# Performance work log

Hardware: AMD Instinct MI355X
Metric: run time of the kernel (lower is better)

## Reference

```python
import math
import jax, jax.numpy as jnp
import numpy as np
from jax.scipy.special import erf

BATCH, SEQ, DIM = 2, 4096, 128
EMA_HEADS, DQK, DV = 16, 64, 256
NUM_BUCKETS, MAX_DIST = 32, 128


def _next_fast_len(n):
    # smallest 5-smooth integer >= n (matches scipy.fftpack.next_fast_len)
    while True:
        m = n
        for p in (2, 3, 5):
            while m % p == 0:
                m //= p
        if m == 1:
            return n
        n += 1


def _laplacian_attn(x):
    mu = math.sqrt(0.5)
    std = math.sqrt(0.25 * math.pi)
    return 0.5 * (1.0 + erf((x - mu) / (std * math.sqrt(2.0))))


def _rel_pos_bias(table, n, scale):
    # causal T5 relative position bias, bucket(q_pos - k_pos)
    pos = jnp.arange(n)
    rel = jnp.maximum(pos[:, None] - pos[None, :], 0)  # [n, n], >= 0
    max_exact = NUM_BUCKETS // 2
    is_small = rel < max_exact
    val_large = max_exact + (
        jnp.log(jnp.maximum(rel, 1).astype(jnp.float32) / max_exact)
        / math.log(MAX_DIST / max_exact) * (NUM_BUCKETS - max_exact)
    ).astype(jnp.int32)
    val_large = jnp.minimum(val_large, NUM_BUCKETS - 1)
    bucket = jnp.where(is_small, rel, val_large)
    return table[bucket, 0] * scale  # [n, n]


def _conv1d_fft(x, K, n):
    # x: [b, n, h, d] (fft over axis 1), K: [n, h] (fft over axis 0)
    fast_len = _next_fast_len(2 * n - 1)
    f_x = jnp.fft.rfft(x, n=fast_len, axis=1)
    f_K = jnp.fft.rfft(K, n=fast_len, axis=0)
    out = jnp.fft.irfft(f_x * jnp.conj(f_K)[None, :, :, None], fast_len, axis=1)
    out = jnp.roll(out, -1, axis=1)
    return out[:, fast_len - n:]  # [b, n, h, d]


def _forward(x, expansion, reduction, alphas, dampen, Wqk, bqk, gamma, beta,
             Wv, bv, rel_table, Wr, br, Wu, bu, Wh, Uh, bh):
    b, n, d = x.shape
    # ---- multi-headed EMA (causal -> unidirectional) via FFT conv ----
    xe = jnp.einsum('bnd,hd->bnhd', x, expansion)
    a = jax.nn.sigmoid(alphas)            # [h]
    dm = jax.nn.sigmoid(dampen)           # [h]
    powers = jnp.arange(n - 1, -1, -1, dtype=x.dtype)  # reversed powers
    K = a * ((1.0 - a) * dm) ** powers[:, None]        # [n, h]
    conv = _conv1d_fft(xe, K, n)
    ema = jnp.einsum('bnhd,hd->bnd', conv, reduction)  # [b, n, d]
    # ---- single-headed attention (chunk_size=-1 -> one chunk), v from x ----
    qk = jax.nn.silu(ema @ Wqk + bqk)     # [b, n, dqk]
    q = qk * gamma[0] + beta[0]
    k = qk * gamma[1] + beta[1]
    v = jax.nn.silu(x @ Wv + bv)          # [b, n, dv]
    scale = 1.0 / n                       # laplacian_attn_fn scaling
    sim = jnp.einsum('bid,bjd->bij', q, k) * scale
    sim = sim + _rel_pos_bias(rel_table, n, DQK ** 0.5)
    attn = _laplacian_attn(sim)
    causal_mask = jnp.triu(jnp.ones((n, n), dtype=bool), 1)
    attn = jnp.where(causal_mask, 0.0, attn)  # laplacian: zero after activation
    attn_out = jnp.einsum('bij,bjd->bid', attn, v)  # [b, n, dv]
    # ---- gating + output ----
    reset_gate = jax.nn.silu(ema @ Wr + br)         # [b, n, dv]
    update_gate = jax.nn.sigmoid(ema @ Wu + bu)     # [b, n, d]
    gated = attn_out * reset_gate
    H = jax.nn.silu(ema @ Wh + gated @ Uh + bh)     # [b, n, d]
    return update_gate * H + (1.0 - update_gate) * x


def setup_inputs() -> dict:
    key = jax.random.key(0)
    ks = jax.random.split(key, 18)
    def rn(i, shape, s=1.0):
        return jax.random.normal(ks[i], shape, dtype=jnp.float32) * s
    return dict(
        x=rn(0, (BATCH, SEQ, DIM)),
        expansion=rn(1, (EMA_HEADS, DIM), 0.2),
        reduction=rn(2, (EMA_HEADS, DIM), 0.2),
        alphas=rn(3, (EMA_HEADS,)),
        dampen=rn(4, (EMA_HEADS,)),
        Wqk=rn(5, (DIM, DQK), 0.05), bqk=rn(6, (DQK,), 0.02),
        gamma=rn(7, (2, DQK), 0.02), beta=jnp.zeros((2, DQK), jnp.float32),
        Wv=rn(8, (DIM, DV), 0.05), bv=rn(9, (DV,), 0.02),
        rel_table=rn(10, (NUM_BUCKETS, 1), 0.02),
        Wr=rn(11, (DIM, DV), 0.05), br=rn(12, (DV,), 0.02),
        Wu=rn(13, (DIM, DIM), 0.05), bu=rn(14, (DIM,), 0.02),
        Wh=rn(15, (DIM, DIM), 0.05), Uh=rn(16, (DV, DIM), 0.05),
        bh=rn(17, (DIM,), 0.02),
    )


def reference(x, expansion, reduction, alphas, dampen, Wqk, bqk, gamma, beta,
              Wv, bv, rel_table, Wr, br, Wu, bu, Wh, Uh, bh):
    return _forward(x, expansion, reduction, alphas, dampen, Wqk, bqk, gamma,
                    beta, Wv, bv, rel_table, Wr, br, Wu, bu, Wh, Uh, bh)
```

## Files before the change

### kernel.cpp

```cpp
#include <hip/hip_runtime.h>
#include <cstdint>
#include <cmath>

#define B_ 2
#define N_ 4096
#define D_ 128
#define H_ 16
#define DQK_ 64
#define DV_ 256

typedef float    f4_t  __attribute__((ext_vector_type(4)));
typedef float    f16f  __attribute__((ext_vector_type(16)));
typedef _Float16 h4_t  __attribute__((ext_vector_type(4)));
typedef _Float16 h8_t  __attribute__((ext_vector_type(8)));

__device__ __forceinline__ float sigmoidf_(float z) { return 1.f/(1.f + expf(-z)); }
__device__ __forceinline__ float siluf_(float z)    { return z/(1.f + expf(-z)); }
__device__ __forceinline__ f16f zero16() {
  f16f z;
#pragma unroll
  for (int i = 0; i < 16; ++i) z[i] = 0.f;
  return z;
}

__global__ void ema_phase1(const float* __restrict__ x, const float* __restrict__ expansion,
                           const float* __restrict__ alphas, const float* __restrict__ dampen,
                           float* __restrict__ F, _Float16* __restrict__ xh) {
  int bid = blockIdx.x;
  int dg = bid & 7, c = (bid >> 3) & 63, b = bid >> 9;
  int h = threadIdx.x & 15, dl = threadIdx.x >> 4;
  int d = dg*16 + dl;
  float a  = sigmoidf_(alphas[h]);
  float dm = sigmoidf_(dampen[h]);
  float q  = (1.f - a)*dm;
  float coef = a * expansion[h*D_ + d];
  __shared__ float xs[64][16];
  {
    int e = threadIdx.x;
    int t = e >> 2, seg = e & 3;
    const float* xp = x + ((size_t)b*N_ + c*64 + t)*D_ + dg*16 + seg*4;
    f4_t v = *(const f4_t*)xp;
    *(f4_t*)&xs[t][seg*4] = v;
    h4_t hv;
#pragma unroll
    for (int j = 0; j < 4; ++j) hv[j] = (_Float16)v[j];
    *(h4_t*)(xh + ((size_t)b*N_ + c*64 + t)*D_ + dg*16 + seg*4) = hv;
  }
  __syncthreads();
  float s = 0.f;
#pragma unroll
  for (int t = 0; t < 64; ++t) s = fmaf(q, s, coef*xs[t][dl]);
  F[(((size_t)b*H_ + h)*D_ + d)*64 + c] = s;
}

__global__ void ema_carry(const float* __restrict__ F, const float* __restrict__ alphas,
                          const float* __restrict__ dampen, float* __restrict__ carry) {
  int idx = blockIdx.x*256 + threadIdx.x;
  int h = (idx >> 7) & 15;
  float a  = sigmoidf_(alphas[h]);
  float dm = sigmoidf_(dampen[h]);
  float q  = (1.f - a)*dm;
  float qL = q;
#pragma unroll
  for (int i = 0; i < 6; ++i) qL *= qL;
  const float* Fp = F + (size_t)idx*64;
  float* cp = carry + (size_t)idx*64;
  float s = 0.f;
  for (int cc = 0; cc < 64; ++cc) { cp[cc] = s; s = fmaf(qL, s, Fp[cc]); }
}

__global__ void ema_phase2(const float* __restrict__ x, const float* __restrict__ expansion,
                           const float* __restrict__ reduction,
                           const float* __restrict__ alphas, const float* __restrict__ dampen,
                           const float* __restrict__ carry, _Float16* __restrict__ emah) {
  int bid = blockIdx.x;
  int dg = bid & 7, c = (bid >> 3) & 63, b = bid >> 9;
  int h = threadIdx.x & 15, dl = threadIdx.x >> 4;
  int d = dg*16 + dl;
  float a  = sigmoidf_(alphas[h]);
  float dm = sigmoidf_(dampen[h]);
  float q  = (1.f - a)*dm;
  float coef = a * expansion[h*D_ + d];
  float red  = reduction[h*D_ + d];
  __shared__ float xs[64][16];
  {
    int e = threadIdx.x;
    int t = e >> 2, seg = e & 3;
    const float* xp = x + ((size_t)b*N_ + c*64 + t)*D_ + dg*16 + seg*4;
    *(f4_t*)&xs[t][seg*4] = *(const f4_t*)xp;
  }
  __syncthreads();
  float s = carry[(((size_t)b*H_ + h)*D_ + d)*64 + c];
  for (int t = 0; t < 64; ++t) {
    s = fmaf(q, s, coef*xs[t][dl]);
    float v = red * s;
    v += __shfl_xor(v, 1); v += __shfl_xor(v, 2);
    v += __shfl_xor(v, 4); v += __shfl_xor(v, 8);
    if (h == 0) emah[((size_t)b*N_ + c*64 + t)*D_ + d] = (_Float16)v;
  }
}

__global__ void prep_all(const float* __restrict__ Wqk, const float* __restrict__ Wv,
                         const float* __restrict__ Wr, const float* __restrict__ Wu,
                         const float* __restrict__ Wh,
                         const float* __restrict__ bqk, const float* __restrict__ bv,
                         const float* __restrict__ br, const float* __restrict__ bu,
                         const float* __restrict__ bh,
                         const float* __restrict__ Uh, const float* __restrict__ rel_table,
                         _Float16* __restrict__ Wt, float* __restrict__ bcat,
                         _Float16* __restrict__ Uht, float* __restrict__ bias2T) {
  int idx = blockIdx.x*256 + threadIdx.x;
  if (idx < 832*128) {
    int c = idx >> 7, d = idx & 127;
    const float* W; const float* bias; int ncol, cl;
    if (c < 64)       { W=Wqk; bias=bqk; ncol=64;  cl=c; }
    else if (c < 320) { W=Wv;  bias=bv;  ncol=256; cl=c-64; }
    else if (c < 576) { W=Wr;  bias=br;  ncol=256; cl=c-320; }
    else if (c < 704) { W=Wu;  bias=bu;  ncol=128; cl=c-576; }
    else              { W=Wh;  bias=bh;  ncol=128; cl=c-704; }
    Wt[idx] = (_Float16)W[d*ncol + cl];
    if (d == 0) bcat[c] = bias[cl];
  } else if (idx < 832*128 + 32768) {
    int i2 = idx - 832*128;
    int k = i2 >> 7, c = i2 & 127;
    Uht[(size_t)c*256 + k] = (_Float16)Uh[i2];
  } else if (idx < 832*128 + 32768 + 4096) {
    int r = idx - (832*128 + 32768);
    int bucket;
    if (r < 16) bucket = r;
    else {
      double v = log((double)r / 16.0) / log(8.0) * 16.0;
      bucket = 16 + (int)v;
      if (bucket > 31) bucket = 31;
    }
    bias2T[r] = (rel_table[bucket]*8.0f - 0.70710678f) * 1.1283792f;
  }
}

__global__ __launch_bounds__(256) void linear_mfma(
    const _Float16* __restrict__ emah, const _Float16* __restrict__ xh,
    const _Float16* __restrict__ Wt, const float* __restrict__ bcat,
    const float* __restrict__ gamma, const float* __restrict__ beta,
    _Float16* __restrict__ qh, _Float16* __restrict__ kh, _Float16* __restrict__ vTt,
    float* __restrict__ resetb, float* __restrict__ updateb, float* __restrict__ hemab) {
  int slab = blockIdx.x % 13, rt = blockIdx.x / 13;
  int tid = threadIdx.x;
  int lane = tid & 63, w = tid >> 6;
  int lr = lane & 15, lg = lane >> 4;
  int mode = (slab==0)?0:(slab<5)?1:(slab<9)?2:(slab<11)?3:4;
  const _Float16* src = (mode==1) ? xh : emah;
  __shared__ _Float16 As[64][136];
  __shared__ _Float16 Ws[64][136];
  {
    const h8_t* s8 = (const h8_t*)(src + (size_t)rt*64*D_);
#pragma unroll
    for (int i = 0; i < 4; ++i) {
      int idx = tid + i*256;
      int row = idx >> 4, seg = idx & 15;
      *(h8_t*)&As[row][seg*8] = s8[idx];
    }
    const h8_t* w8 = (const h8_t*)(Wt + (size_t)slab*64*D_);
#pragma unroll
    for (int i = 0; i < 4; ++i) {
      int idx = tid + i*256;
      int row = idx >> 4, seg = idx & 15;
      *(h8_t*)&Ws[row][seg*8] = w8[idx];
    }
  }
  __syncthreads();
  h4_t af[8];
#pragma unroll
  for (int ks = 0; ks < 8; ++ks) af[ks] = *(const h4_t*)&As[w*16 + lr][ks*16 + lg*4];
  int row0 = rt*64 + w*16 + lg*4;
#pragma unroll
  for (int ns = 0; ns < 4; ++ns) {
    f4_t acc = (f4_t){0.f,0.f,0.f,0.f};
#pragma unroll
    for (int ks = 0; ks < 8; ++ks) {
      h4_t bf = *(const h4_t*)&Ws[ns*16 + lr][ks*16 + lg*4];
      acc = __builtin_amdgcn_mfma_f32_16x16x16f16(af[ks], bf, acc, 0, 0, 0);
    }
    int c = slab*64 + ns*16 + lr;
    float bias = bcat[c];
    if (mode == 0) {
      float g0 = gamma[c], g1 = gamma[64+c], be0 = beta[c], be1 = beta[64+c];
#pragma unroll
      for (int r = 0; r < 4; ++r) {
        float qk = siluf_(acc[r] + bias);
        size_t row = row0 + r;
        qh[row*DQK_ + c] = (_Float16)(qk*g0 + be0);
        kh[row*DQK_ + c] = (_Float16)(qk*g1 + be1);
      }
    } else if (mode == 1) {
      int cl = c - 64;
      int bb = row0 >> 12, rl = row0 & 4095;
      h4_t vv;
#pragma unroll
      for (int r = 0; r < 4; ++r) vv[r] = (_Float16)siluf_(acc[r] + bias);
      *(h4_t*)&vTt[(((size_t)bb*128 + (rl>>5))*256 + cl)*32 + (rl&31)] = vv;
    } else if (mode == 2) {
      int cl = c - 320;
#pragma unroll
      for (int r = 0; r < 4; ++r) resetb[(size_t)(row0 + r)*DV_ + cl] = siluf_(acc[r] + bias);
    } else if (mode == 3) {
      int cl = c - 576;
#pragma unroll
      for (int r = 0; r < 4; ++r) updateb[(size_t)(row0 + r)*D_ + cl] = sigmoidf_(acc[r] + bias);
    } else {
      int cl = c - 704;
#pragma unroll
      for (int r = 0; r < 4; ++r) hemab[(size_t)(row0 + r)*D_ + cl] = acc[r] + bias;
    }
  }
}

__global__ __launch_bounds__(256, 3) void attn_kernel(
    const _Float16* __restrict__ qh, const _Float16* __restrict__ kh,
    const _Float16* __restrict__ vTt, const float* __restrict__ bias2T,
    _Float16* __restrict__ attnp) {
  int bid = blockIdx.x;
  int it = 63 - (bid >> 5);
  int rem = bid & 31;
  int s = rem >> 1, b = rem & 1;
  int a = it >> 2, r = it & 3;
  int nblk = a + 1;
  if (s >= nblk) return;
  int T = 2*it + 2;
  int tlo = (s*T)/nblk, thi = ((s+1)*T)/nblk;
  int nt = thi - tlo;
  int base = it + 2*a*(a-1) + r*a;
  int slot = base + s;
  int i0 = it * 64;
  int tid = threadIdx.x;
  int lane = tid & 63, w = tid >> 6;
  int ih = w & 1;
  int dvh = w >> 1;
  bool prod = (dvh == 0);
  int lm = lane & 31, lg = lane >> 5;

  __shared__ __align__(16) char Vb[2][18432];
  __shared__ __align__(16) char Kb[2][4352];
  __shared__ __align__(16) char Pb[2][2560];
  __shared__ float biasW[320];

  int jmaxv = thi*32 - 1;
  int dlo = i0 - jmaxv;
  int cnt = 64 + jmaxv - tlo*32;
  for (int k = tid; k < cnt; k += 256) {
    int d = dlo + k;
    biasW[k] = d < 0 ? -1e38f : bias2T[d];
  }

  h4_t qf[8];
  if (prod) {
    const _Float16* qp = qh + ((size_t)b*N_ + i0 + ih*32 + lm)*DQK_ + 4*lg;
#pragma unroll
    for (int ksq = 0; ksq < 8; ++ksq) qf[ksq] = *(const h4_t*)(qp + 8*ksq);
  }

  f16f accO[4];
#pragma unroll
  for (int i = 0; i < 4; ++i) accO[i] = zero16();

  const _Float16* kbase = kh + (size_t)b*N_*DQK_;
  const _Float16* vbase = vTt + (size_t)b*128*8192;
  int st = tid & 127;
  int kr = st >> 2, ks16 = st & 3;

  h8_t k8a, k8b, vr[8];
#define ISSUE_(JT) { \
  const _Float16* kp_ = kbase + (size_t)((JT)*32 + kr)*DQK_ + ks16*16; \
  k8a = *(const h8_t*)kp_; k8b = *(const h8_t*)(kp_ + 8); \
  const _Float16* vp_ = vbase + (size_t)(JT)*8192 + st*32; \
  _Pragma("unroll") for (int i = 0; i < 4; ++i) vr[i] = *(const h8_t*)(vp_ + i*8); \
  _Pragma("unroll") for (int i = 0; i < 4; ++i) vr[4+i] = *(const h8_t*)(vp_ + 4096 + i*8); }

#define COMMIT_(BI) { \
  char* kb_ = Kb[BI] + kr*136 + ks16*32; \
  *(h4_t*)kb_        = __builtin_shufflevector(k8a, k8a, 0,1,2,3); \
  *(h4_t*)(kb_ + 8)  = __builtin_shufflevector(k8a, k8a, 4,5,6,7); \
  *(h4_t*)(kb_ + 16) = __builtin_shufflevector(k8b, k8b, 0,1,2,3); \
  *(h4_t*)(kb_ + 24) = __builtin_shufflevector(k8b, k8b, 4,5,6,7); \
  char* va_ = Vb[BI] + st*72; \
  _Pragma("unroll") for (int i = 0; i < 4; ++i) { \
    *(h4_t*)(va_ + i*16)     = __builtin_shufflevector(vr[i], vr[i], 0,1,2,3); \
    *(h4_t*)(va_ + i*16 + 8) = __builtin_shufflevector(vr[i], vr[i], 4,5,6,7); } \
  char* vb2_ = Vb[BI] + (st + 128)*72; \
  _Pragma("unroll") for (int i = 0; i < 4; ++i) { \
    *(h4_t*)(vb2_ + i*16)     = __builtin_shufflevector(vr[4+i], vr[4+i], 0,1,2,3); \
    *(h4_t*)(vb2_ + i*16 + 8) = __builtin_shufflevector(vr[4+i], vr[4+i], 4,5,6,7); } }

  if (!prod) {
    ISSUE_(tlo);
    COMMIT_(0);
    if (nt > 1) ISSUE_(tlo + 1);
  }
  __syncthreads();

  const float C1 = 1.1283792f / 4096.f;
  int ibase = i0 + ih*32 + lm;
#pragma unroll 1
  for (int t = 0; t < nt; ++t) {
    h4_t pa[4];
    if (prod) {
      const char* kb = Kb[t & 1];
      __builtin_amdgcn_s_setprio(1);
      f16f accS = zero16();
#pragma unroll
      for (int ksq = 0; ksq < 8; ++ksq) {
        h4_t kf = *(const h4_t*)(kb + lm*136 + 16*ksq + 8*lg);
        accS = __builtin_amdgcn_mfma_f32_32x32x8f16(kf, qf[ksq], accS, 0, 0, 0);
      }
      __builtin_amdgcn_s_setprio(0);
      int idx0 = ibase - dlo - (tlo + t)*32 - 4*lg;
#pragma unroll
      for (int rr = 0; rr < 16; ++rr) {
        float tt = fmaf(accS[rr], C1, biasW[idx0 - 8*(rr>>2) - (rr&3)]);
        float e = tt*fmaf(tt*tt, -0.101797f, -2.304877f);
        float u = exp2f(e);
        float pv = __builtin_amdgcn_rcpf(1.f + u);
        pa[rr>>2][rr&3] = (_Float16)pv;
      }
      char* pp = Pb[ih] + lane*40;
#pragma unroll
      for (int k2 = 0; k2 < 4; ++k2) *(h4_t*)(pp + k2*8) = pa[k2];
    } else {
      if (t+1 < nt) COMMIT_((t+1) & 1);
      if (t+2 < nt) ISSUE_(tlo + t + 2);
    }
    __syncthreads();
    if (!prod) {
      const char* pp = Pb[ih] + lane*40;
#pragma unroll
      for (int k2 = 0; k2 < 4; ++k2) pa[k2] = *(const h4_t*)(pp + k2*8);
    }
    const char* vb = Vb[t & 1];
    __builtin_amdgcn_s_setprio(1);
#pragma unroll
    for (int ks = 0; ks < 4; ++ks) {
#pragma unroll
      for (int dvb = 0; dvb < 4; ++dvb) {
        h4_t vf = *(const h4_t*)(vb + (dvh*128 + dvb*32 + lm)*72 + 16*ks + 8*lg);
        accO[dvb] = __builtin_amdgcn_mfma_f32_32x32x8f16(pa[ks], vf, accO[dvb], 0, 0, 0);
      }
    }
    __builtin_amdgcn_s_setprio(0);
    __syncthreads();
  }
#undef ISSUE_
#undef COMMIT_

  _Float16* op = attnp + ((size_t)b*544 + slot)*(64*256);
#pragma unroll
  for (int dvb = 0; dvb < 4; ++dvb) {
    int col = dvh*128 + dvb*32 + lm;
#pragma unroll
    for (int rr = 0; rr < 16; ++rr) {
      int row = ih*32 + 8*(rr>>2) + 4*lg + (rr&3);
      op[(size_t)row*256 + col] = (_Float16)accO[dvb][rr];
    }
  }
}

__global__ void combine_gated(const _Float16* __restrict__ attnp, const float* __restrict__ resetb,
                              _Float16* __restrict__ gatedh) {
  size_t fi = (size_t)blockIdx.x*256 + threadIdx.x;
  int c4 = (int)(fi & 63);
  int rr = (int)(fi >> 6);
  int b = rr >> 12, n = rr & 4095;
  int it = n >> 6, rowLocal = n & 63;
  int a = it >> 2, r = it & 3;
  int nblk = a + 1;
  int base = it + 2*a*(a-1) + r*a;
  const _Float16* ap = attnp + ((size_t)b*544 + base)*16384 + rowLocal*256 + c4*4;
  f4_t acc = (f4_t){0.f,0.f,0.f,0.f};
  for (int s2 = 0; s2 < nblk; ++s2) {
    h4_t pv = *(const h4_t*)(ap + (size_t)s2*16384);
#pragma unroll
    for (int j = 0; j < 4; ++j) acc[j] += (float)pv[j];
  }
  f4_t rg = ((const f4_t*)resetb)[fi];
  f4_t g = acc * rg;
  h4_t hg;
#pragma unroll
  for (int j = 0; j < 4; ++j) hg[j] = (_Float16)g[j];
  *(h4_t*)(gatedh + fi*4) = hg;
}

__global__ __launch_bounds__(256) void final_mfma(
    const _Float16* __restrict__ gatedh, const _Float16* __restrict__ Uht,
    const float* __restrict__ hemab, const float* __restrict__ updateb,
    const float* __restrict__ x, float* __restrict__ out) {
  int rt = blockIdx.x >> 1, cs = blockIdx.x & 1;
  int tid = threadIdx.x;
  int lane = tid & 63, w = tid >> 6;
  int lr = lane & 15, lg = lane >> 4;
  int row0 = rt*64, c0 = cs*64;
  __shared__ _Float16 As[64][136];
  __shared__ _Float16 Ws[64][136];
  f4_t acc[4];
#pragma unroll
  for (int ns = 0; ns < 4; ++ns) acc[ns] = (f4_t){0.f,0.f,0.f,0.f};
#pragma unroll
  for (int kc = 0; kc < 2; ++kc) {
    __syncthreads();
#pragma unroll
    for (int i = 0; i < 4; ++i) {
      int idx = tid + i*256;
      int row = idx >> 4, seg = idx & 15;
      *(h8_t*)&As[row][seg*8] =
          *(const h8_t*)(gatedh + (size_t)(row0 + row)*DV_ + kc*128 + seg*8);
      *(h8_t*)&Ws[row][seg*8] =
          *(const h8_t*)(Uht + (size_t)(c0 + row)*DV_ + kc*128 + seg*8);
    }
    __syncthreads();
    h4_t af[8];
#pragma unroll
    for (int ks = 0; ks < 8; ++ks) af[ks] = *(const h4_t*)&As[w*16 + lr][ks*16 + lg*4];
#pragma unroll
    for (int ns = 0; ns < 4; ++ns) {
#pragma unroll
      for (int ks = 0; ks < 8; ++ks) {
        h4_t bf = *(const h4_t*)&Ws[ns*16 + lr][ks*16 + lg*4];
        acc[ns] = __builtin_amdgcn_mfma_f32_16x16x16f16(af[ks], bf, acc[ns], 0, 0, 0);
      }
    }
  }
  int orow = row0 + w*16 + lg*4;
#pragma unroll
  for (int ns = 0; ns < 4; ++ns) {
    int col = c0 + ns*16 + lr;
#pragma unroll
    for (int r = 0; r < 4; ++r) {
      size_t o = (size_t)(orow + r)*D_ + col;
      float z = acc[ns][r] + hemab[o];
      float Hv = siluf_(z);
      float u  = updateb[o];
      out[o] = u*Hv + (1.f - u)*x[o];
    }
  }
}

extern "C" void kernel_launch(void* const* d_in, const int* in_sizes, int n_in,
                              void* d_out, int out_size, void* d_ws, size_t ws_size,
                              hipStream_t stream) {
  (void)in_sizes; (void)n_in; (void)out_size; (void)ws_size;
  const float* x         = (const float*)d_in[0];
  const float* expansion = (const float*)d_in[1];
  const float* reduction = (const float*)d_in[2];
  const float* alphas    = (const float*)d_in[3];
  const float* dampen    = (const float*)d_in[4];
  const float* Wqk       = (const float*)d_in[5];
  const float* bqk       = (const float*)d_in[6];
  const float* gamma     = (const float*)d_in[7];
  const float* beta      = (const float*)d_in[8];
  const float* Wv        = (const float*)d_in[9];
  const float* bv        = (const float*)d_in[10];
  const float* rel_table = (const float*)d_in[11];
  const float* Wr        = (const float*)d_in[12];
  const float* br        = (const float*)d_in[13];
  const float* Wu        = (const float*)d_in[14];
  const float* bu        = (const float*)d_in[15];
  const float* Wh        = (const float*)d_in[16];
  const float* Uh        = (const float*)d_in[17];
  const float* bh        = (const float*)d_in[18];
  float* out = (float*)d_out;

  char* p = (char*)d_ws;
  size_t off = 0;
  auto alloc = [&](size_t bytes) -> char* {
    char* r = p + off;
    off += (bytes + 255) & ~(size_t)255;
    return r;
  };
  float*    F      = (float*)alloc((size_t)B_*H_*D_*64*4);
  float*    carry  = (float*)alloc((size_t)B_*H_*D_*64*4);
  _Float16* emah   = (_Float16*)alloc((size_t)B_*N_*D_*2);
  _Float16* xh     = (_Float16*)alloc((size_t)B_*N_*D_*2);
  float*    bias2T = (float*)alloc((size_t)N_*4);
  _Float16* Wt     = (_Float16*)alloc((size_t)832*128*2);
  float*    bcat   = (float*)alloc((size_t)832*4);
  _Float16* Uht    = (_Float16*)alloc((size_t)D_*DV_*2);
  _Float16* qh     = (_Float16*)alloc((size_t)B_*N_*DQK_*2);
  _Float16* kh     = (_Float16*)alloc((size_t)B_*N_*DQK_*2);
  _Float16* vTt    = (_Float16*)alloc((size_t)B_*DV_*N_*2);
  float*    resetb = (float*)alloc((size_t)B_*N_*DV_*4);
  float*    updateb= (float*)alloc((size_t)B_*N_*D_*4);
  float*    hemab  = (float*)alloc((size_t)B_*N_*D_*4);
  _Float16* gatedh = (_Float16*)alloc((size_t)B_*N_*DV_*2);
  _Float16* attnp  = (_Float16*)alloc((size_t)B_*544*64*256*2);

  prep_all<<<560, 256, 0, stream>>>(Wqk, Wv, Wr, Wu, Wh, bqk, bv, br, bu, bh,
                                    Uh, rel_table, Wt, bcat, Uht, bias2T);
  ema_phase1<<<1024, 256, 0, stream>>>(x, expansion, alphas, dampen, F, xh);
  ema_carry<<<16, 256, 0, stream>>>(F, alphas, dampen, carry);
  ema_phase2<<<1024, 256, 0, stream>>>(x, expansion, reduction, alphas, dampen, carry, emah);
  linear_mfma<<<128*13, 256, 0, stream>>>(emah, xh, Wt, bcat, gamma, beta,
                                          qh, kh, vTt, resetb, updateb, hemab);
  attn_kernel<<<2048, 256, 0, stream>>>(qh, kh, vTt, bias2T, attnp);
  combine_gated<<<2048, 256, 0, stream>>>(attnp, resetb, gatedh);
  final_mfma<<<256, 256, 0, stream>>>(gatedh, Uht, hemab, updateb, x, out);
}
```

Measured before the change: 113.8 us.

## Parallelize EMA carry with warp scan; store reset/update gates as fp16

The sequential per-thread carry recurrence over 64 chunks, run on only 16 blocks, is replaced by a wave-level Hillis-Steele scan over the affine recurrence, launched on 1024 blocks with one wave per (b,h,d) row. This removes a long serial dependency chain with low occupancy. Separately, the reset and update gate buffers are stored in fp16 instead of fp32, halving their write and read traffic in linear_mfma, combine_gated and final_mfma. The cost is some precision loss in the gate values and a different summation order in the carry.

```diff
diff --git a/kernel.cpp b/kernel.cpp
--- a/kernel.cpp
+++ b/kernel.cpp
@@ -55,18 +55,25 @@
 
 __global__ void ema_carry(const float* __restrict__ F, const float* __restrict__ alphas,
                           const float* __restrict__ dampen, float* __restrict__ carry) {
-  int idx = blockIdx.x*256 + threadIdx.x;
-  int h = (idx >> 7) & 15;
+  int wid = blockIdx.x*4 + (threadIdx.x >> 6);
+  int lane = threadIdx.x & 63;
+  int h = (wid >> 7) & 15;
   float a  = sigmoidf_(alphas[h]);
   float dm = sigmoidf_(dampen[h]);
   float q  = (1.f - a)*dm;
   float qL = q;
 #pragma unroll
   for (int i = 0; i < 6; ++i) qL *= qL;
-  const float* Fp = F + (size_t)idx*64;
-  float* cp = carry + (size_t)idx*64;
-  float s = 0.f;
-  for (int cc = 0; cc < 64; ++cc) { cp[cc] = s; s = fmaf(qL, s, Fp[cc]); }
+  float A = qL;
+  float Bv = F[(size_t)wid*64 + lane];
+#pragma unroll
+  for (int len = 1; len < 64; len <<= 1) {
+    float Ap = __shfl_up(A, len);
+    float Bp = __shfl_up(Bv, len);
+    if (lane >= len) { Bv = fmaf(A, Bp, Bv); A = A*Ap; }
+  }
+  float Bprev = __shfl_up(Bv, 1);
+  carry[(size_t)wid*64 + lane] = (lane == 0) ? 0.f : Bprev;
 }
 
 __global__ void ema_phase2(const float* __restrict__ x, const float* __restrict__ expansion,
@@ -142,7 +149,8 @@
     const _Float16* __restrict__ Wt, const float* __restrict__ bcat,
     const float* __restrict__ gamma, const float* __restrict__ beta,
     _Float16* __restrict__ qh, _Float16* __restrict__ kh, _Float16* __restrict__ vTt,
-    float* __restrict__ resetb, float* __restrict__ updateb, float* __restrict__ hemab) {
+    _Float16* __restrict__ resetbh, _Float16* __restrict__ updatebh,
+    float* __restrict__ hemab) {
   int slab = blockIdx.x % 13, rt = blockIdx.x / 13;
   int tid = threadIdx.x;
   int lane = tid & 63, w = tid >> 6;
@@ -201,11 +209,13 @@
     } else if (mode == 2) {
       int cl = c - 320;
 #pragma unroll
-      for (int r = 0; r < 4; ++r) resetb[(size_t)(row0 + r)*DV_ + cl] = siluf_(acc[r] + bias);
+      for (int r = 0; r < 4; ++r)
+        resetbh[(size_t)(row0 + r)*DV_ + cl] = (_Float16)siluf_(acc[r] + bias);
     } else if (mode == 3) {
       int cl = c - 576;
 #pragma unroll
-      for (int r = 0; r < 4; ++r) updateb[(size_t)(row0 + r)*D_ + cl] = sigmoidf_(acc[r] + bias);
+      for (int r = 0; r < 4; ++r)
+        updatebh[(size_t)(row0 + r)*D_ + cl] = (_Float16)sigmoidf_(acc[r] + bias);
     } else {
       int cl = c - 704;
 #pragma unroll
@@ -362,7 +372,8 @@
   }
 }
 
-__global__ void combine_gated(const _Float16* __restrict__ attnp, const float* __restrict__ resetb,
+__global__ void combine_gated(const _Float16* __restrict__ attnp,
+                              const _Float16* __restrict__ resetbh,
                               _Float16* __restrict__ gatedh) {
   size_t fi = (size_t)blockIdx.x*256 + threadIdx.x;
   int c4 = (int)(fi & 63);
@@ -379,17 +390,16 @@
 #pragma unroll
     for (int j = 0; j < 4; ++j) acc[j] += (float)pv[j];
   }
-  f4_t rg = ((const f4_t*)resetb)[fi];
-  f4_t g = acc * rg;
+  h4_t rg = *(const h4_t*)(resetbh + fi*4);
   h4_t hg;
 #pragma unroll
-  for (int j = 0; j < 4; ++j) hg[j] = (_Float16)g[j];
+  for (int j = 0; j < 4; ++j) hg[j] = (_Float16)(acc[j] * (float)rg[j]);
   *(h4_t*)(gatedh + fi*4) = hg;
 }
 
 __global__ __launch_bounds__(256) void final_mfma(
     const _Float16* __restrict__ gatedh, const _Float16* __restrict__ Uht,
-    const float* __restrict__ hemab, const float* __restrict__ updateb,
+    const float* __restrict__ hemab, const _Float16* __restrict__ updatebh,
     const float* __restrict__ x, float* __restrict__ out) {
   int rt = blockIdx.x >> 1, cs = blockIdx.x & 1;
   int tid = threadIdx.x;
@@ -435,7 +445,7 @@
       size_t o = (size_t)(orow + r)*D_ + col;
       float z = acc[ns][r] + hemab[o];
       float Hv = siluf_(z);
-      float u  = updateb[o];
+      float u  = (float)updatebh[o];
       out[o] = u*Hv + (1.f - u)*x[o];
     }
   }
@@ -473,31 +483,31 @@
     off += (bytes + 255) & ~(size_t)255;
     return r;
   };
-  float*    F      = (float*)alloc((size_t)B_*H_*D_*64*4);
-  float*    carry  = (float*)alloc((size_t)B_*H_*D_*64*4);
-  _Float16* emah   = (_Float16*)alloc((size_t)B_*N_*D_*2);
-  _Float16* xh     = (_Float16*)alloc((size_t)B_*N_*D_*2);
-  float*    bias2T = (float*)alloc((size_t)N_*4);
-  _Float16* Wt     = (_Float16*)alloc((size_t)832*128*2);
-  float*    bcat   = (float*)alloc((size_t)832*4);
-  _Float16* Uht    = (_Float16*)alloc((size_t)D_*DV_*2);
-  _Float16* qh     = (_Float16*)alloc((size_t)B_*N_*DQK_*2);
-  _Float16* kh     = (_Float16*)alloc((size_t)B_*N_*DQK_*2);
-  _Float16* vTt    = (_Float16*)alloc((size_t)B_*DV_*N_*2);
-  float*    resetb = (float*)alloc((size_t)B_*N_*DV_*4);
-  float*    updateb= (float*)alloc((size_t)B_*N_*D_*4);
-  float*    hemab  = (float*)alloc((size_t)B_*N_*D_*4);
-  _Float16* gatedh = (_Float16*)alloc((size_t)B_*N_*DV_*2);
-  _Float16* attnp  = (_Float16*)alloc((size_t)B_*544*64*256*2);
+  float*    F       = (float*)alloc((size_t)B_*H_*D_*64*4);
+  float*    carry   = (float*)alloc((size_t)B_*H_*D_*64*4);
+  _Float16* emah    = (_Float16*)alloc((size_t)B_*N_*D_*2);
+  _Float16* xh      = (_Float16*)alloc((size_t)B_*N_*D_*2);
+  float*    bias2T  = (float*)alloc((size_t)N_*4);
+  _Float16* Wt      = (_Float16*)alloc((size_t)832*128*2);
+  float*    bcat    = (float*)alloc((size_t)832*4);
+  _Float16* Uht     = (_Float16*)alloc((size_t)D_*DV_*2);
+  _Float16* qh      = (_Float16*)alloc((size_t)B_*N_*DQK_*2);
+  _Float16* kh      = (_Float16*)alloc((size_t)B_*N_*DQK_*2);
+  _Float16* vTt     = (_Float16*)alloc((size_t)B_*DV_*N_*2);
+  _Float16* resetbh = (_Float16*)alloc((size_t)B_*N_*DV_*2);
+  _Float16* updatebh= (_Float16*)alloc((size_t)B_*N_*D_*2);
+  float*    hemab   = (float*)alloc((size_t)B_*N_*D_*4);
+  _Float16* gatedh  = (_Float16*)alloc((size_t)B_*N_*DV_*2);
+  _Float16* attnp   = (_Float16*)alloc((size_t)B_*544*64*256*2);
 
   prep_all<<<560, 256, 0, stream>>>(Wqk, Wv, Wr, Wu, Wh, bqk, bv, br, bu, bh,
                                     Uh, rel_table, Wt, bcat, Uht, bias2T);
   ema_phase1<<<1024, 256, 0, stream>>>(x, expansion, alphas, dampen, F, xh);
-  ema_carry<<<16, 256, 0, stream>>>(F, alphas, dampen, carry);
+  ema_carry<<<1024, 256, 0, stream>>>(F, alphas, dampen, carry);
   ema_phase2<<<1024, 256, 0, stream>>>(x, expansion, reduction, alphas, dampen, carry, emah);
   linear_mfma<<<128*13, 256, 0, stream>>>(emah, xh, Wt, bcat, gamma, beta,
-                                          qh, kh, vTt, resetb, updateb, hemab);
+                                          qh, kh, vTt, resetbh, updatebh, hemab);
   attn_kernel<<<2048, 256, 0, stream>>>(qh, kh, vTt, bias2T, attnp);
-  combine_gated<<<2048, 256, 0, stream>>>(attnp, resetb, gatedh);
-  final_mfma<<<256, 256, 0, stream>>>(gatedh, Uht, hemab, updateb, x, out);
-}
+  combine_gated<<<2048, 256, 0, stream>>>(attnp, resetbh, gatedh);
+  final_mfma<<<256, 256, 0, stream>>>(gatedh, Uht, hemab, updatebh, x, out);
+}
```

Measured after the change: 108.7 us. 1.05x faster.
